# Kernel optimization log

Hardware: AMD Instinct MI355X
Metric: run time of the kernel (lower is better)

## Reference

```python
import jax, jax.numpy as jnp
import numpy as np

B, S, DM, H, HD = 2, 4096, 768, 12, 64   # longformer-base-4096
W = 256    # one-sided attention window (attention_window=512)
NB = S // W
G = 16     # number of leading global-attention tokens ([CLS]+query)
OUT = 512  # hidden_dim of final fc


def setup_inputs() -> dict:
    key = jax.random.key(0)
    ks = jax.random.split(key, 11)
    def w(k, shape):
        return jax.random.normal(k, shape, jnp.float32) * 0.02
    z = lambda n: jnp.zeros((n,), jnp.float32)
    return {
        "x": jax.random.normal(ks[0], (B, S, DM), jnp.float32),
        "wq": w(ks[1], (DM, DM)), "bq": z(DM),
        "wk": w(ks[2], (DM, DM)), "bk": z(DM),
        "wv": w(ks[3], (DM, DM)), "bv": z(DM),
        "wqg": w(ks[4], (DM, DM)), "bqg": z(DM),
        "wkg": w(ks[5], (DM, DM)), "bkg": z(DM),
        "wvg": w(ks[6], (DM, DM)), "bvg": z(DM),
        "wo": w(ks[7], (DM, DM)), "bo": z(DM),
        "wp": w(ks[8], (DM, DM)), "bp": z(DM),
        "wfc": w(ks[9], (DM, OUT)), "bfc": z(OUT),
    }


def _longformer_forward(x, wq, bq, wk, bk, wv, bv, wqg, bqg, wkg, bkg,
                        wvg, bvg, wo, bo, wp, bp, wfc, bfc):
    scale = jnp.float32(1.0 / np.sqrt(HD))
    q = ((x @ wq + bq) * scale).reshape(B, S, H, HD)
    k = (x @ wk + bk).reshape(B, S, H, HD)
    v = (x @ wv + bv).reshape(B, S, H, HD)

    # --- sliding-window (banded) attention via overlapping key/value blocks ---
    kp = jnp.pad(k, ((0, 0), (W, W), (0, 0), (0, 0)))  # [B, S+2W, H, HD]
    vp = jnp.pad(v, ((0, 0), (W, W), (0, 0), (0, 0)))
    blk = jnp.arange(NB)[:, None] * W + jnp.arange(3 * W)[None, :]  # [NB,3W]
    kb = kp[:, blk]  # [B, NB, 3W, H, HD]
    vb = vp[:, blk]
    qb = q.reshape(B, NB, W, H, HD)
    sc_loc = jnp.einsum('bnqhd,bnkhd->bhnqk', qb, kb)  # [B,H,NB,W,3W]

    i = jnp.arange(W)[:, None]
    j = jnp.arange(3 * W)[None, :]
    band = (j >= i) & (j <= i + 2 * W)                       # |rel| <= W
    abs_k = (jnp.arange(NB)[:, None, None] - 1) * W + j[None]  # [NB,W,3W]
    # mask padding, out-of-band, and global keys (handled separately per HF)
    valid = band[None] & (abs_k >= 0) & (abs_k < S) & (abs_k >= G)
    sc_loc = jnp.where(valid[None, None], sc_loc, jnp.float32(-1e9))

    # every query also attends to the G global keys (regular k/v per HF)
    sc_glb = jnp.einsum('bqhd,bghd->bhqg', q, k[:, :G])  # [B,H,S,G]

    sc = jnp.concatenate([sc_glb, sc_loc.reshape(B, H, S, 3 * W)], axis=-1)
    p = jax.nn.softmax(sc, axis=-1)
    p_g, p_l = p[..., :G], p[..., G:]
    out = jnp.einsum('bhqg,bghd->bqhd', p_g, v[:, :G])
    out = out + jnp.einsum('bhnqk,bnkhd->bnqhd',
                           p_l.reshape(B, H, NB, W, 3 * W), vb).reshape(B, S, H, HD)

    # --- global queries: full attention with the dedicated global projections ---
    qg = ((x[:, :G] @ wqg + bqg) * scale).reshape(B, G, H, HD)
    kg = (x @ wkg + bkg).reshape(B, S, H, HD)
    vg = (x @ wvg + bvg).reshape(B, S, H, HD)
    pg = jax.nn.softmax(jnp.einsum('bghd,bshd->bhgs', qg, kg), axis=-1)
    out_g = jnp.einsum('bhgs,bshd->bghd', pg, vg)
    out = jnp.concatenate([out_g, out[:, G:]], axis=1)

    attn = out.reshape(B, S, DM) @ wo + bo
    pooled = jnp.tanh(attn[:, 0] @ wp + bp)  # HF pooler on [CLS]
    return pooled @ wfc + bfc                # final nn.Linear -> [B, OUT]


def reference(x, wq, bq, wk, bk, wv, bv, wqg, bqg, wkg, bkg, wvg, bvg,
              wo, bo, wp, bp, wfc, bfc):
    return _longformer_forward(x, wq, bq, wk, bk, wv, bv, wqg, bqg, wkg,
                               bkg, wvg, bvg, wo, bo, wp, bp, wfc, bfc)
```

## Files before the change

### kernel.cpp

```cpp
#include <hip/hip_runtime.h>
#include <hip/hip_bf16.h>

#define BB 2
#define SS 4096
#define DM 768
#define NH 12
#define OUTC 512
#define QSCALE 0.125f
#define NCHUNK 128
#define CS 32
#define JT 32

__device__ __forceinline__ float wave_sum64(float v) {
#pragma unroll
  for (int o = 32; o > 0; o >>= 1) v += __shfl_xor(v, o, 64);
  return v;
}

__global__ __launch_bounds__(256) void kA(const float* __restrict__ x,
    const float* __restrict__ wqg, const float* __restrict__ bqg,
    const float* __restrict__ wkg, const float* __restrict__ bkg,
    float* __restrict__ qw_ws, float* __restrict__ qb_ws,
    float* __restrict__ l_ws, float* __restrict__ xw_ws) {
  int h = blockIdx.x, b = blockIdx.y, js = blockIdx.z, t = threadIdx.x;
  __shared__ float x0[DM];
  __shared__ float red[4][64];
  __shared__ float qg0[64];
  for (int i = t; i < DM; i += 256) x0[i] = x[(size_t)b*SS*DM + i];
  for (int i = t; i < 384; i += 256)
    xw_ws[((size_t)b*NH + h)*DM + js*384 + i] = 0.f;
  if (js == 0 && t == 0) l_ws[b*NH + h] = 0.f;
  __syncthreads();
  int d = t & 63, g = t >> 6;
  float p = 0.f;
  for (int j = g*192; j < g*192 + 192; ++j)
    p += x0[j] * wqg[(size_t)j*DM + h*64 + d];
  red[g][d] = p;
  __syncthreads();
  if (t < 64)
    qg0[t] = (red[0][t] + red[1][t] + red[2][t] + red[3][t] + bqg[h*64 + t]) * QSCALE;
  __syncthreads();
  if (js == 0 && t == 0) {
    float qb = 0.f;
    for (int dd = 0; dd < 64; ++dd) qb += qg0[dd] * bkg[h*64 + dd];
    qb_ws[b*NH + h] = qb;
  }
  const float4* qg4 = (const float4*)qg0;
  for (int jj = t; jj < 384; jj += 256) {
    int j = js*384 + jj;
    const float4* wr = (const float4*)(wkg + (size_t)j*DM + h*64);
    float acc = 0.f;
#pragma unroll
    for (int q = 0; q < 16; ++q) {
      float4 wv = wr[q], qv = qg4[q];
      acc += wv.x*qv.x + wv.y*qv.y + wv.z*qv.z + wv.w*qv.w;
    }
    qw_ws[((size_t)b*NH + h)*DM + j] = acc;
  }
}

__global__ __launch_bounds__(256) void kB(const float* __restrict__ x,
    const float* __restrict__ qw_ws, const float* __restrict__ qb_ws,
    float* __restrict__ l_ws, float* __restrict__ xw_ws) {
  int chunk = blockIdx.x, b = blockIdx.y;
  int t = threadIdx.x, lane = t & 63, w = t >> 6;
  __shared__ alignas(16) float qw[NH*DM];
  __shared__ float qb[NH];
  __shared__ alignas(16) float pl[CS*NH];
  for (int i = t; i < NH*DM; i += 256) qw[i] = qw_ws[(size_t)b*NH*DM + i];
  if (t < NH) qb[t] = qb_ws[b*NH + t];
  __syncthreads();
  const size_t xbase = ((size_t)b*SS + chunk*CS) * DM;
  const float4* x4 = (const float4*)(x + xbase);
  const float4* qw4 = (const float4*)qw;
  float lacc = 0.f;

  for (int batch = 0; batch < 2; ++batch) {
    int sl = w*8 + batch*4;
    float acc[4][NH];
#pragma unroll
    for (int si = 0; si < 4; ++si)
#pragma unroll
      for (int hh = 0; hh < NH; ++hh) acc[si][hh] = 0.f;
#pragma unroll
    for (int k = 0; k < 3; ++k) {
      int jq = k*64 + lane;
      float4 xf[4];
#pragma unroll
      for (int si = 0; si < 4; ++si)
        xf[si] = x4[(size_t)(sl + si)*192 + jq];
#pragma unroll
      for (int hh = 0; hh < NH; ++hh) {
        float4 qv = qw4[hh*192 + jq];
#pragma unroll
        for (int si = 0; si < 4; ++si)
          acc[si][hh] += xf[si].x*qv.x + xf[si].y*qv.y + xf[si].z*qv.z + xf[si].w*qv.w;
      }
    }
    float preg = 0.f;
#pragma unroll
    for (int si = 0; si < 4; ++si)
#pragma unroll
      for (int hh = 0; hh < NH; ++hh) {
        float r = wave_sum64(acc[si][hh]);
        float pp = __expf(r + qb[hh]);
        if (lane == hh) lacc += pp;
        if (lane == si*NH + hh) preg = pp;
      }
    if (lane < 4*NH) pl[(sl + lane/NH)*NH + (lane % NH)] = preg;
  }
  if (lane < NH) atomicAdd(&l_ws[b*NH + lane], lacc);
  __syncthreads();

  float a2[NH][3];
#pragma unroll
  for (int hh = 0; hh < NH; ++hh)
#pragma unroll
    for (int i = 0; i < 3; ++i) a2[hh][i] = 0.f;
  for (int s = 0; s < CS; ++s) {
    float4 p0 = *(const float4*)(&pl[s*NH + 0]);
    float4 p1 = *(const float4*)(&pl[s*NH + 4]);
    float4 p2 = *(const float4*)(&pl[s*NH + 8]);
    float pv[NH] = {p0.x,p0.y,p0.z,p0.w, p1.x,p1.y,p1.z,p1.w, p2.x,p2.y,p2.z,p2.w};
    float xv[3];
#pragma unroll
    for (int i = 0; i < 3; ++i)
      xv[i] = x[xbase + (size_t)s*DM + t + 256*i];
#pragma unroll
    for (int hh = 0; hh < NH; ++hh)
#pragma unroll
      for (int i = 0; i < 3; ++i) a2[hh][i] += pv[hh]*xv[i];
  }
#pragma unroll
  for (int hh = 0; hh < NH; ++hh)
#pragma unroll
    for (int i = 0; i < 3; ++i)
      atomicAdd(&xw_ws[((size_t)b*NH + hh)*DM + t + 256*i], a2[hh][i]);
}

__global__ __launch_bounds__(256) void kE1(const float* __restrict__ xw_ws,
    const float* __restrict__ l_ws, const float* __restrict__ wvg,
    const float* __restrict__ bvg, float* __restrict__ out0_ws,
    float* __restrict__ zbuf) {
  int h = blockIdx.x, b = blockIdx.y, t = threadIdx.x;
  __shared__ float xws[DM];
  __shared__ float red[4][64];
  int bid = b*NH + h;
  if (t < 128) zbuf[bid*128 + t] = 0.f;
  float inv = 1.f / l_ws[b*NH + h];
  for (int i = 0; i < 3; ++i) {
    int j = t + 256*i;
    xws[j] = xw_ws[((size_t)b*NH + h)*DM + j] * inv;
  }
  __syncthreads();
  int ci = t & 63, g = t >> 6;
  float acc = 0.f;
  for (int j = g*192; j < g*192 + 192; ++j)
    acc += xws[j] * wvg[(size_t)j*DM + h*64 + ci];
  red[g][ci] = acc;
  __syncthreads();
  if (t < 64)
    out0_ws[b*DM + h*64 + t] =
        red[0][t] + red[1][t] + red[2][t] + red[3][t] + bvg[h*64 + t];
}

__global__ __launch_bounds__(192) void kT(const float* __restrict__ inraw,
    const float* __restrict__ bias, const float* __restrict__ W,
    float* __restrict__ outacc) {
  int jb = blockIdx.x, t = threadIdx.x;
  __shared__ float xs[2][DM/JT];
  const int JR = DM/JT;
  int j0 = jb*JR;
  if (t < 2*JR) {
    int bb = t / JR, jj = t % JR;
    float v = inraw[bb*DM + j0 + jj];
    if (bias) v += bias[j0 + jj];
    xs[bb][jj] = v;
  }
  __syncthreads();
  float4 a0 = {0,0,0,0}, a1 = {0,0,0,0};
  const float4* W4 = (const float4*)W;
#pragma unroll 4
  for (int jj = 0; jj < JR; ++jj) {
    float4 wv = W4[(size_t)(j0 + jj)*192 + t];
    float s0 = xs[0][jj], s1 = xs[1][jj];
    a0.x += s0*wv.x; a0.y += s0*wv.y; a0.z += s0*wv.z; a0.w += s0*wv.w;
    a1.x += s1*wv.x; a1.y += s1*wv.y; a1.z += s1*wv.z; a1.w += s1*wv.w;
  }
  int c = t*4;
  atomicAdd(&outacc[c+0], a0.x); atomicAdd(&outacc[c+1], a0.y);
  atomicAdd(&outacc[c+2], a0.z); atomicAdd(&outacc[c+3], a0.w);
  atomicAdd(&outacc[DM+c+0], a1.x); atomicAdd(&outacc[DM+c+1], a1.y);
  atomicAdd(&outacc[DM+c+2], a1.z); atomicAdd(&outacc[DM+c+3], a1.w);
}

__global__ __launch_bounds__(256) void kT3(const float* __restrict__ pooledraw,
    const float* __restrict__ bp, const float* __restrict__ wfc,
    const float* __restrict__ bfc, float* __restrict__ out) {
  int tile = blockIdx.x, b = blockIdx.y, t = threadIdx.x;
  __shared__ float pl[DM];
  __shared__ float red[4][64];
  for (int i = t; i < DM; i += 256) pl[i] = tanhf(pooledraw[b*DM + i] + bp[i]);
  __syncthreads();
  int ci = t & 63, g = t >> 6;
  int c = tile*64 + ci;
  float acc = 0.f;
  for (int j = g*192; j < g*192 + 192; ++j)
    acc += pl[j] * wfc[(size_t)j*OUTC + c];
  red[g][ci] = acc;
  __syncthreads();
  if (t < 64)
    out[(size_t)b*OUTC + tile*64 + t] =
        red[0][t] + red[1][t] + red[2][t] + red[3][t] + bfc[tile*64 + t];
}

extern "C" void kernel_launch(void* const* d_in, const int* in_sizes, int n_in,
                              void* d_out, int out_size, void* d_ws, size_t ws_size,
                              hipStream_t stream) {
  const float* x   = (const float*)d_in[0];
  const float* wqg = (const float*)d_in[7];
  const float* bqg = (const float*)d_in[8];
  const float* wkg = (const float*)d_in[9];
  const float* bkg = (const float*)d_in[10];
  const float* wvg = (const float*)d_in[11];
  const float* bvg = (const float*)d_in[12];
  const float* wo  = (const float*)d_in[13];
  const float* bo  = (const float*)d_in[14];
  const float* wp  = (const float*)d_in[15];
  const float* bp  = (const float*)d_in[16];
  const float* wfc = (const float*)d_in[17];
  const float* bfc = (const float*)d_in[18];

  float* ws        = (float*)d_ws;
  float* qw        = ws;
  float* qb        = ws + 18432;
  float* l         = ws + 18456;
  float* xw        = ws + 18480;
  float* out0      = ws + 36912;
  float* attnraw   = ws + 38448;
  float* pooledraw = ws + 39984;

  kA <<<dim3(NH, BB, 2),  256, 0, stream>>>(x, wqg, bqg, wkg, bkg, qw, qb, l, xw);
  kB <<<dim3(NCHUNK, BB), 256, 0, stream>>>(x, qw, qb, l, xw);
  kE1<<<dim3(NH, BB),     256, 0, stream>>>(xw, l, wvg, bvg, out0, attnraw);
  kT <<<dim3(JT),         192, 0, stream>>>(out0, nullptr, wo, attnraw);
  kT <<<dim3(JT),         192, 0, stream>>>(attnraw, bo, wp, pooledraw);
  kT3<<<dim3(8, BB),      256, 0, stream>>>(pooledraw, bp, wfc, bfc, (float*)d_out);
}
```

Measured before the change: 199.4 us.

## Split global-query pipeline into wider kernels and replace atomics with partial-sum reduction

The fused projection kernel is split into three stages (partial q projection, q finalize, key-weight fold), each launched over more blocks. The heavily contended per-chunk atomicAdd accumulation in the main scan is replaced by per-chunk partial buffers plus a separate reduction kernel, and the chunk count is chosen from the available workspace size. The value projection and the small dense layers are spread over more blocks, and the final fc uses 512 threads. The intent is to remove atomic contention and raise occupancy in the small latency-bound stages. The cost is more kernel launches and a large partial-sum buffer that must be written and read back.

```diff
diff --git a/kernel.cpp b/kernel.cpp
--- a/kernel.cpp
+++ b/kernel.cpp
@@ -7,9 +7,6 @@
 #define NH 12
 #define OUTC 512
 #define QSCALE 0.125f
-#define NCHUNK 128
-#define CS 32
-#define JT 32
 
 __device__ __forceinline__ float wave_sum64(float v) {
 #pragma unroll
@@ -17,51 +14,61 @@
   return v;
 }
 
-__global__ __launch_bounds__(256) void kA(const float* __restrict__ x,
-    const float* __restrict__ wqg, const float* __restrict__ bqg,
-    const float* __restrict__ wkg, const float* __restrict__ bkg,
-    float* __restrict__ qw_ws, float* __restrict__ qb_ws,
-    float* __restrict__ l_ws, float* __restrict__ xw_ws) {
+__global__ __launch_bounds__(256) void kQ(const float* __restrict__ x,
+    const float* __restrict__ wqg, float* __restrict__ qpart) {
   int h = blockIdx.x, b = blockIdx.y, js = blockIdx.z, t = threadIdx.x;
-  __shared__ float x0[DM];
+  __shared__ float x0[96];
   __shared__ float red[4][64];
-  __shared__ float qg0[64];
-  for (int i = t; i < DM; i += 256) x0[i] = x[(size_t)b*SS*DM + i];
-  for (int i = t; i < 384; i += 256)
-    xw_ws[((size_t)b*NH + h)*DM + js*384 + i] = 0.f;
-  if (js == 0 && t == 0) l_ws[b*NH + h] = 0.f;
+  if (t < 96) x0[t] = x[(size_t)b*SS*DM + js*96 + t];
   __syncthreads();
   int d = t & 63, g = t >> 6;
-  float p = 0.f;
-  for (int j = g*192; j < g*192 + 192; ++j)
-    p += x0[j] * wqg[(size_t)j*DM + h*64 + d];
-  red[g][d] = p;
+  float acc = 0.f;
+  for (int k = 0; k < 24; ++k) {
+    int j = js*96 + g*24 + k;
+    acc += x0[g*24 + k] * wqg[(size_t)j*DM + h*64 + d];
+  }
+  red[g][d] = acc;
   __syncthreads();
   if (t < 64)
-    qg0[t] = (red[0][t] + red[1][t] + red[2][t] + red[3][t] + bqg[h*64 + t]) * QSCALE;
-  __syncthreads();
-  if (js == 0 && t == 0) {
-    float qb = 0.f;
-    for (int dd = 0; dd < 64; ++dd) qb += qg0[dd] * bkg[h*64 + dd];
-    qb_ws[b*NH + h] = qb;
-  }
-  const float4* qg4 = (const float4*)qg0;
-  for (int jj = t; jj < 384; jj += 256) {
-    int j = js*384 + jj;
-    const float4* wr = (const float4*)(wkg + (size_t)j*DM + h*64);
-    float acc = 0.f;
-#pragma unroll
-    for (int q = 0; q < 16; ++q) {
-      float4 wv = wr[q], qv = qg4[q];
-      acc += wv.x*qv.x + wv.y*qv.y + wv.z*qv.z + wv.w*qv.w;
-    }
-    qw_ws[((size_t)b*NH + h)*DM + j] = acc;
-  }
-}
-
+    qpart[(((size_t)b*NH + h)*8 + js)*64 + t] =
+        red[0][t] + red[1][t] + red[2][t] + red[3][t];
+}
+
+__global__ __launch_bounds__(64) void kQf(const float* __restrict__ qpart,
+    const float* __restrict__ bqg, const float* __restrict__ bkg,
+    float* __restrict__ qg_ws, float* __restrict__ qb_ws, float* __restrict__ l_ws) {
+  int h = blockIdx.x, b = blockIdx.y, t = threadIdx.x;
+  float s = 0.f;
+#pragma unroll
+  for (int js = 0; js < 8; ++js)
+    s += qpart[(((size_t)b*NH + h)*8 + js)*64 + t];
+  float qg = (s + bqg[h*64 + t]) * QSCALE;
+  qg_ws[((size_t)b*NH + h)*64 + t] = qg;
+  float qb = wave_sum64(qg * bkg[h*64 + t]);
+  if (t == 0) { qb_ws[b*NH + h] = qb; l_ws[b*NH + h] = 0.f; }
+}
+
+__global__ __launch_bounds__(192) void kAp(const float* __restrict__ qg_ws,
+    const float* __restrict__ wkg, float* __restrict__ qw_ws) {
+  int h = blockIdx.x, b = blockIdx.y, js = blockIdx.z, t = threadIdx.x;
+  __shared__ float4 qg4[16];
+  if (t < 16) qg4[t] = ((const float4*)qg_ws)[((size_t)b*NH + h)*16 + t];
+  __syncthreads();
+  int j = js*192 + t;
+  const float4* wr = (const float4*)wkg + (size_t)j*192 + h*16;
+  float acc = 0.f;
+#pragma unroll
+  for (int q = 0; q < 16; ++q) {
+    float4 wv = wr[q], qv = qg4[q];
+    acc += wv.x*qv.x + wv.y*qv.y + wv.z*qv.z + wv.w*qv.w;
+  }
+  qw_ws[((size_t)b*NH + h)*DM + j] = acc;
+}
+
+template<int CS>
 __global__ __launch_bounds__(256) void kB(const float* __restrict__ x,
     const float* __restrict__ qw_ws, const float* __restrict__ qb_ws,
-    float* __restrict__ l_ws, float* __restrict__ xw_ws) {
+    float* __restrict__ l_ws, float* __restrict__ part, int nchunk) {
   int chunk = blockIdx.x, b = blockIdx.y;
   int t = threadIdx.x, lane = t & 63, w = t >> 6;
   __shared__ alignas(16) float qw[NH*DM];
@@ -70,13 +77,14 @@
   for (int i = t; i < NH*DM; i += 256) qw[i] = qw_ws[(size_t)b*NH*DM + i];
   if (t < NH) qb[t] = qb_ws[b*NH + t];
   __syncthreads();
-  const size_t xbase = ((size_t)b*SS + chunk*CS) * DM;
+  const size_t xbase = ((size_t)b*SS + (size_t)chunk*CS) * DM;
   const float4* x4 = (const float4*)(x + xbase);
   const float4* qw4 = (const float4*)qw;
   float lacc = 0.f;
 
-  for (int batch = 0; batch < 2; ++batch) {
-    int sl = w*8 + batch*4;
+#pragma unroll
+  for (int batch = 0; batch < CS/16; ++batch) {
+    int sl = w*(CS/4) + batch*4;
     float acc[4][NH];
 #pragma unroll
     for (int si = 0; si < 4; ++si)
@@ -131,45 +139,45 @@
 #pragma unroll
       for (int i = 0; i < 3; ++i) a2[hh][i] += pv[hh]*xv[i];
   }
+  float* dst = part + ((size_t)(b*nchunk + chunk)*NH)*DM;
 #pragma unroll
   for (int hh = 0; hh < NH; ++hh)
 #pragma unroll
-    for (int i = 0; i < 3; ++i)
-      atomicAdd(&xw_ws[((size_t)b*NH + hh)*DM + t + 256*i], a2[hh][i]);
-}
-
-__global__ __launch_bounds__(256) void kE1(const float* __restrict__ xw_ws,
-    const float* __restrict__ l_ws, const float* __restrict__ wvg,
-    const float* __restrict__ bvg, float* __restrict__ out0_ws,
-    float* __restrict__ zbuf) {
-  int h = blockIdx.x, b = blockIdx.y, t = threadIdx.x;
-  __shared__ float xws[DM];
-  __shared__ float red[4][64];
-  int bid = b*NH + h;
-  if (t < 128) zbuf[bid*128 + t] = 0.f;
-  float inv = 1.f / l_ws[b*NH + h];
-  for (int i = 0; i < 3; ++i) {
-    int j = t + 256*i;
-    xws[j] = xw_ws[((size_t)b*NH + h)*DM + j] * inv;
-  }
-  __syncthreads();
-  int ci = t & 63, g = t >> 6;
-  float acc = 0.f;
-  for (int j = g*192; j < g*192 + 192; ++j)
-    acc += xws[j] * wvg[(size_t)j*DM + h*64 + ci];
-  red[g][ci] = acc;
-  __syncthreads();
-  if (t < 64)
-    out0_ws[b*DM + h*64 + t] =
-        red[0][t] + red[1][t] + red[2][t] + red[3][t] + bvg[h*64 + t];
+    for (int i = 0; i < 3; ++i) dst[hh*DM + t + 256*i] = a2[hh][i];
+}
+
+__global__ __launch_bounds__(192) void kR(const float* __restrict__ part,
+    const float* __restrict__ l_ws, float* __restrict__ xwn,
+    float* __restrict__ zbuf, int nchunk) {
+  int js = blockIdx.x, h = blockIdx.y, b = blockIdx.z, t = threadIdx.x;
+  int bid = ((b*NH + h)*4 + js);
+  for (int k = t; k < 48; k += 192) zbuf[bid*48 + k] = 0.f;
+  int j = js*192 + t;
+  float s = 0.f;
+  for (int c = 0; c < nchunk; ++c)
+    s += part[((size_t)(b*nchunk + c)*NH + h)*DM + j];
+  xwn[((size_t)b*NH + h)*DM + j] = s / l_ws[b*NH + h];
+}
+
+__global__ __launch_bounds__(64) void kE1p(const float* __restrict__ xwn,
+    const float* __restrict__ wvg, float* __restrict__ out0acc) {
+  int js = blockIdx.x, h = blockIdx.y, b = blockIdx.z, t = threadIdx.x;
+  __shared__ float xs[64];
+  xs[t] = xwn[((size_t)b*NH + h)*DM + js*64 + t];
+  __syncthreads();
+  float acc = 0.f;
+#pragma unroll 8
+  for (int jj = 0; jj < 64; ++jj)
+    acc += xs[jj] * wvg[(size_t)(js*64 + jj)*DM + h*64 + t];
+  atomicAdd(&out0acc[b*DM + h*64 + t], acc);
 }
 
 __global__ __launch_bounds__(192) void kT(const float* __restrict__ inraw,
     const float* __restrict__ bias, const float* __restrict__ W,
     float* __restrict__ outacc) {
   int jb = blockIdx.x, t = threadIdx.x;
-  __shared__ float xs[2][DM/JT];
-  const int JR = DM/JT;
+  const int JR = 12;
+  __shared__ float xs[2][JR];
   int j0 = jb*JR;
   if (t < 2*JR) {
     int bb = t / JR, jj = t % JR;
@@ -180,7 +188,7 @@
   __syncthreads();
   float4 a0 = {0,0,0,0}, a1 = {0,0,0,0};
   const float4* W4 = (const float4*)W;
-#pragma unroll 4
+#pragma unroll
   for (int jj = 0; jj < JR; ++jj) {
     float4 wv = W4[(size_t)(j0 + jj)*192 + t];
     float s0 = xs[0][jj], s1 = xs[1][jj];
@@ -194,24 +202,28 @@
   atomicAdd(&outacc[DM+c+2], a1.z); atomicAdd(&outacc[DM+c+3], a1.w);
 }
 
-__global__ __launch_bounds__(256) void kT3(const float* __restrict__ pooledraw,
+__global__ __launch_bounds__(512) void kT3(const float* __restrict__ pooledraw,
     const float* __restrict__ bp, const float* __restrict__ wfc,
     const float* __restrict__ bfc, float* __restrict__ out) {
   int tile = blockIdx.x, b = blockIdx.y, t = threadIdx.x;
   __shared__ float pl[DM];
-  __shared__ float red[4][64];
-  for (int i = t; i < DM; i += 256) pl[i] = tanhf(pooledraw[b*DM + i] + bp[i]);
-  __syncthreads();
-  int ci = t & 63, g = t >> 6;
-  int c = tile*64 + ci;
-  float acc = 0.f;
-  for (int j = g*192; j < g*192 + 192; ++j)
-    acc += pl[j] * wfc[(size_t)j*OUTC + c];
-  red[g][ci] = acc;
-  __syncthreads();
-  if (t < 64)
-    out[(size_t)b*OUTC + tile*64 + t] =
-        red[0][t] + red[1][t] + red[2][t] + red[3][t] + bfc[tile*64 + t];
+  __shared__ float red[8][64];
+  for (int i = t; i < DM; i += 512) pl[i] = tanhf(pooledraw[b*DM + i] + bp[i]);
+  __syncthreads();
+  int c = t & 63, jg = t >> 6;
+  float acc = 0.f;
+  for (int jj = 0; jj < 96; ++jj) {
+    int j = jg*96 + jj;
+    acc += pl[j] * wfc[(size_t)j*OUTC + tile*64 + c];
+  }
+  red[jg][c] = acc;
+  __syncthreads();
+  if (t < 64) {
+    float r = bfc[tile*64 + t];
+#pragma unroll
+    for (int g = 0; g < 8; ++g) r += red[g][t];
+    out[(size_t)b*OUTC + tile*64 + t] = r;
+  }
 }
 
 extern "C" void kernel_launch(void* const* d_in, const int* in_sizes, int n_in,
@@ -232,18 +244,30 @@
   const float* bfc = (const float*)d_in[18];
 
   float* ws        = (float*)d_ws;
-  float* qw        = ws;
-  float* qb        = ws + 18432;
-  float* l         = ws + 18456;
-  float* xw        = ws + 18480;
-  float* out0      = ws + 36912;
-  float* attnraw   = ws + 38448;
-  float* pooledraw = ws + 39984;
-
-  kA <<<dim3(NH, BB, 2),  256, 0, stream>>>(x, wqg, bqg, wkg, bkg, qw, qb, l, xw);
-  kB <<<dim3(NCHUNK, BB), 256, 0, stream>>>(x, qw, qb, l, xw);
-  kE1<<<dim3(NH, BB),     256, 0, stream>>>(xw, l, wvg, bvg, out0, attnraw);
-  kT <<<dim3(JT),         192, 0, stream>>>(out0, nullptr, wo, attnraw);
-  kT <<<dim3(JT),         192, 0, stream>>>(attnraw, bo, wp, pooledraw);
-  kT3<<<dim3(8, BB),      256, 0, stream>>>(pooledraw, bp, wfc, bfc, (float*)d_out);
-}
+  float* qpart     = ws;
+  float* qg        = ws + 12288;
+  float* qb        = ws + 13824;
+  float* l         = ws + 13848;
+  float* qw        = ws + 13872;
+  float* xwn       = ws + 32304;
+  float* out0acc   = ws + 50736;
+  float* attnraw   = ws + 52272;
+  float* pooledraw = ws + 53808;
+  float* part      = ws + 55360;
+
+  size_t need128 = (55360 + (size_t)2*128*NH*DM) * 4;
+  int nchunk = (ws_size >= need128) ? 128 : 64;
+
+  kQ  <<<dim3(NH, BB, 8), 256, 0, stream>>>(x, wqg, qpart);
+  kQf <<<dim3(NH, BB),     64, 0, stream>>>(qpart, bqg, bkg, qg, qb, l);
+  kAp <<<dim3(NH, BB, 4), 192, 0, stream>>>(qg, wkg, qw);
+  if (nchunk == 128)
+    kB<32><<<dim3(128, BB), 256, 0, stream>>>(x, qw, qb, l, part, 128);
+  else
+    kB<64><<<dim3(64,  BB), 256, 0, stream>>>(x, qw, qb, l, part, 64);
+  kR  <<<dim3(4, NH, BB), 192, 0, stream>>>(part, l, xwn, out0acc, nchunk);
+  kE1p<<<dim3(12, NH, BB), 64, 0, stream>>>(xwn, wvg, out0acc);
+  kT  <<<dim3(64),        192, 0, stream>>>(out0acc, bvg, wo, attnraw);
+  kT  <<<dim3(64),        192, 0, stream>>>(attnraw,  bo, wp, pooledraw);
+  kT3 <<<dim3(8, BB),     512, 0, stream>>>(pooledraw, bp, wfc, bfc, (float*)d_out);
+}
```

Result: slower. 220.1 us (+10.4%).
